# Performance work log

Measured on AMD Instinct MI355X. Metric: run time of the kernel, lower is better.

Reference implementation:

```python
import jax, jax.numpy as jnp
import numpy as np

N_NODES = 100_000
N_EDGES = 1_250_000
IN_FEATS, N_HIDDEN, N_CLASSES = 64, 64, 32


def setup_inputs() -> dict:
    key = jax.random.key(0)
    ks = jax.random.split(key, 8)
    x = jax.random.normal(ks[0], (N_NODES, IN_FEATS), dtype=jnp.float32)
    src = jax.random.randint(ks[1], (N_EDGES,), 0, N_NODES, dtype=jnp.int64)
    dst = jax.random.randint(ks[2], (N_EDGES,), 0, N_NODES, dtype=jnp.int64)
    s1 = 1.0 / np.sqrt(IN_FEATS)
    s2 = 1.0 / np.sqrt(N_HIDDEN)
    W_self1 = jax.random.normal(ks[3], (IN_FEATS, N_HIDDEN), dtype=jnp.float32) * s1
    W_neigh1 = jax.random.normal(ks[4], (IN_FEATS, N_HIDDEN), dtype=jnp.float32) * s1
    b1 = jnp.zeros((N_HIDDEN,), dtype=jnp.float32)
    W_self2 = jax.random.normal(ks[5], (N_HIDDEN, N_CLASSES), dtype=jnp.float32) * s2
    W_neigh2 = jax.random.normal(ks[6], (N_HIDDEN, N_CLASSES), dtype=jnp.float32) * s2
    b2 = jnp.zeros((N_CLASSES,), dtype=jnp.float32)
    return dict(x=x, src=src, dst=dst, W_self1=W_self1, W_neigh1=W_neigh1, b1=b1,
                W_self2=W_self2, W_neigh2=W_neigh2, b2=b2)


def _sage_conv(h, src, dst, W_self, W_neigh, b):
    # mean aggregation over in-neighbors: gather src feats, segment-sum by dst
    n = h.shape[0]
    msg = h[src]  # [E, d] -- dominant memory traffic
    agg = jax.ops.segment_sum(msg, dst, num_segments=n)
    deg = jax.ops.segment_sum(jnp.ones_like(dst, dtype=h.dtype), dst, num_segments=n)
    h_neigh = agg / jnp.maximum(deg, 1.0)[:, None]  # zero-degree nodes get 0 (DGL behavior)
    return h @ W_self + h_neigh @ W_neigh + b


def reference(x, src, dst, W_self1, W_neigh1, b1, W_self2, W_neigh2, b2):
    h = _sage_conv(x, src, dst, W_self1, W_neigh1, b1)
    h = jax.nn.relu(h)
    # dropout(p=0.5) is identity in eval mode
    return _sage_conv(h, src, dst, W_self2, W_neigh2, b2)
```

## Files before the change

### kernel.cpp

```cpp
#include <hip/hip_runtime.h>
#include <hip/hip_bf16.h>


#define NF 64
#define BW 256
#define BSH 8
#define MAXB 512
#define CAPMAX 8192
#define P1_CHUNK 2048
#define H1S 68

typedef __attribute__((ext_vector_type(8))) short short8;
typedef __attribute__((ext_vector_type(8))) unsigned short ushort8v;
typedef __attribute__((ext_vector_type(4))) float floatx4;

__device__ __forceinline__ short bf16hi(float v) {
    __hip_bfloat16 h = __float2bfloat16(v);
    return *(short*)&h;
}
__device__ __forceinline__ float bf2f(short s) {
    __hip_bfloat16 h = *(__hip_bfloat16*)&s;
    return __bfloat162float(h);
}
__device__ __forceinline__ float bits2f(unsigned short u) {
    unsigned int x = ((unsigned int)u) << 16;
    union { unsigned int i; float f; } c; c.i = x; return c.f;
}


__global__ __launch_bounds__(256) void prep_kernel(
        int* __restrict__ gcursor,
        const float* __restrict__ Ws1, const float* __restrict__ Wn1,
        const float* __restrict__ Ws2, const float* __restrict__ Wn2,
        unsigned short* __restrict__ w1p, unsigned short* __restrict__ w2p) {
    const int tid = threadIdx.x;
    if (blockIdx.x == 0) {
        for (int i = tid; i < MAXB; i += 256) gcursor[i] = 0;
        return;
    }
    const int part = blockIdx.x - 1;
    for (int i = tid; i < 32 * 64; i += 256) {
        int n = part * 32 + (i >> 6), k = i & 63;
        float v = (n < 64) ? Ws1[k * 64 + n] : Wn1[k * 64 + (n - 64)];
        short hv = bf16hi(v);
        w1p[n * 64 + k] = (unsigned short)hv;
        w1p[8192 + n * 64 + k] = (unsigned short)bf16hi(v - bf2f(hv));
    }
    for (int i = tid; i < 16 * 64; i += 256) {
        int n = part * 16 + (i >> 6), k = i & 63;
        float v = (n < 32) ? Ws2[k * 32 + n] : Wn2[k * 32 + (n - 32)];
        short hv = bf16hi(v);
        w2p[n * 64 + k] = (unsigned short)hv;
        w2p[4096 + n * 64 + k] = (unsigned short)bf16hi(v - bf2f(hv));
    }
}


__global__ __launch_bounds__(256) void p1_dense1_kernel(
        const int* __restrict__ src, const int* __restrict__ dst,
        int* __restrict__ gcursor, unsigned* __restrict__ bucket,
        int E, int nbuckets, int dblocks,
        const float* __restrict__ X,
        const unsigned short* __restrict__ w1p,
        const float* __restrict__ bias,
        float* __restrict__ outA,
        unsigned short* __restrict__ outB,
        int N) {
    __shared__ int smem_i[2 * MAXB];
    const int tid = threadIdx.x;

    if ((int)blockIdx.x >= dblocks) {
        int* cnt   = smem_i;
        int* cbase = smem_i + MAXB;
        const int bid = blockIdx.x - dblocks;
        const int beg = bid * P1_CHUNK;
        const int end = min(E, beg + P1_CHUNK);
        for (int i = tid; i < nbuckets; i += 256) cnt[i] = 0;
        __syncthreads();
        for (int e = beg + tid; e < end; e += 256)
            atomicAdd(&cnt[dst[e] >> BSH], 1);
        __syncthreads();
        for (int i = tid; i < nbuckets; i += 256) {
            int c = cnt[i];
            cbase[i] = c ? atomicAdd(&gcursor[i], c) : 0;
            cnt[i] = 0;
        }
        __syncthreads();
        for (int e = beg + tid; e < end; e += 256) {
            int d = dst[e];
            int r = d >> BSH;
            int p = cbase[r] + atomicAdd(&cnt[r], 1);
            if (p < CAPMAX)
                bucket[(size_t)r * CAPMAX + p] = ((unsigned)src[e] << BSH) | (unsigned)(d & (BW - 1));
        }
        return;
    }

    constexpr int NT = 8, NSELF = 4;
    const int lane = tid & 63;
    const int wid  = tid >> 6;
    const int m = lane & 15, quad = lane >> 4;
    const int rowblk = blockIdx.x * 128 + wid * 32;

    floatx4 acc[2][NT];
    #pragma unroll
    for (int rt = 0; rt < 2; ++rt)
        #pragma unroll
        for (int t = 0; t < NT; ++t) acc[rt][t] = (floatx4)(0.f);

    short8 ah[2][2], al[2][2];
    #pragma unroll
    for (int rt = 0; rt < 2; ++rt) {
        int r = rowblk + rt * 16 + m;
        if (r >= N) r = N - 1;
        const float* xp = X + (size_t)r * 64 + quad * 8;
        #pragma unroll
        for (int h = 0; h < 2; ++h) {
            floatx4 f0 = *(const floatx4*)(xp + h * 32);
            floatx4 f1 = *(const floatx4*)(xp + h * 32 + 4);
            short8 hi, lo;
            #pragma unroll
            for (int j = 0; j < 4; ++j) {
                short hv = bf16hi(f0[j]);
                hi[j] = hv; lo[j] = bf16hi(f0[j] - bf2f(hv));
                short hv2 = bf16hi(f1[j]);
                hi[4 + j] = hv2; lo[4 + j] = bf16hi(f1[j] - bf2f(hv2));
            }
            ah[rt][h] = hi; al[rt][h] = lo;
        }
    }

    #pragma unroll
    for (int t = 0; t < NT; ++t) {
        int n = t * 16 + m;
        const unsigned short* ph = w1p + n * 64 + quad * 8;
        const unsigned short* pl = ph + 8192;
        #pragma unroll
        for (int h = 0; h < 2; ++h) {
            short8 bh = *(const short8*)(ph + h * 32);
            short8 bl = *(const short8*)(pl + h * 32);
            #pragma unroll
            for (int rt = 0; rt < 2; ++rt) {
                acc[rt][t] = __builtin_amdgcn_mfma_f32_16x16x32_bf16(ah[rt][h], bh, acc[rt][t], 0, 0, 0);
                acc[rt][t] = __builtin_amdgcn_mfma_f32_16x16x32_bf16(al[rt][h], bh, acc[rt][t], 0, 0, 0);
                acc[rt][t] = __builtin_amdgcn_mfma_f32_16x16x32_bf16(ah[rt][h], bl, acc[rt][t], 0, 0, 0);
            }
        }
    }

    #pragma unroll
    for (int rt = 0; rt < 2; ++rt) {
        #pragma unroll
        for (int t = 0; t < NT; ++t) {
            #pragma unroll
            for (int r4 = 0; r4 < 4; ++r4) {
                int row = rowblk + rt * 16 + quad * 4 + r4;
                if (row < N) {
                    if (t < NSELF) {
                        int col = t * 16 + m;
                        outA[(size_t)row * 64 + col] = acc[rt][t][r4] + bias[col];
                    } else {
                        int col = (t - NSELF) * 16 + m;
                        outB[(size_t)row * 64 + col] = (unsigned short)bf16hi(acc[rt][t][r4]);
                    }
                }
            }
        }
    }
}


__global__ __launch_bounds__(256) void p2_csr_kernel(const unsigned* __restrict__ bucket,
                                                     const int* __restrict__ gcursor,
                                                     int* __restrict__ row_start,
                                                     int* __restrict__ csr_src,
                                                     int N, int nbuckets) {
    __shared__ unsigned stage[CAPMAX];
    __shared__ int cnt[BW];
    __shared__ int excl[BW];
    const int r = blockIdx.x;
    const int tid = threadIdx.x;

    int partial = 0;
    for (int i = tid; i < r; i += 256) partial += min(gcursor[i], CAPMAX);
    excl[tid] = partial;
    __syncthreads();
    for (int off = 128; off > 0; off >>= 1) {
        if (tid < off) excl[tid] += excl[tid + off];
        __syncthreads();
    }
    const int base = excl[0];
    const int sz = min(gcursor[r], CAPMAX);
    const unsigned* bsrc = bucket + (size_t)r * CAPMAX;
    __syncthreads();

    cnt[tid] = 0;
    __syncthreads();
    for (int i = tid; i < sz; i += 256) {
        unsigned v = bsrc[i];
        stage[i] = v;
        atomicAdd(&cnt[v & (BW - 1)], 1);
    }
    __syncthreads();
    excl[tid] = cnt[tid];
    __syncthreads();
    for (int off = 1; off < BW; off <<= 1) {
        int v0 = (tid >= off) ? excl[tid - off] : 0;
        __syncthreads();
        excl[tid] += v0;
        __syncthreads();
    }
    int node = r * BW + tid;
    if (node < N) row_start[node] = base + excl[tid] - cnt[tid];
    if (r == nbuckets - 1 && tid == 0) row_start[N] = base + sz;
    __syncthreads();
    cnt[tid] = excl[tid] - cnt[tid];
    __syncthreads();
    for (int i = tid; i < sz; i += 256) {
        unsigned v = stage[i];
        int p = atomicAdd(&cnt[v & (BW - 1)], 1);
        csr_src[base + p] = (int)(v >> BSH);
    }
}


__global__ __launch_bounds__(256) void agg64_d2_kernel(
        const unsigned short* __restrict__ t1n,
        const float* __restrict__ xs,
        const int* __restrict__ row_start,
        const int* __restrict__ csr_src,
        const unsigned short* __restrict__ w2p,
        const float* __restrict__ b2,
        float* __restrict__ outD,
        unsigned short* __restrict__ t2n,
        int N, int E) {
    __shared__ float h1s[16][H1S];
    const int tid = threadIdx.x;
    const int lane = tid & 63;
    const int wid  = tid >> 6;
    const int half = lane >> 5;
    const int g = (lane >> 3) & 3;
    const int c = lane & 7;
    const int nbase = blockIdx.x * 16;

    const int ln0 = wid * 4 + half;
    const int ln1 = ln0 + 2;
    const int n0 = nbase + ln0, n1 = nbase + ln1;
    int beg0 = 0, end0 = 0, beg1 = 0, end1 = 0;
    if (n0 < N) { beg0 = row_start[n0]; end0 = row_start[n0 + 1]; }
    if (n1 < N) { beg1 = row_start[n1]; end1 = row_start[n1 + 1]; }

    float a0[8] = {0.f, 0.f, 0.f, 0.f, 0.f, 0.f, 0.f, 0.f};
    float a1[8] = {0.f, 0.f, 0.f, 0.f, 0.f, 0.f, 0.f, 0.f};
    int j0 = beg0 + g, j1 = beg1 + g;
    const int Em1 = E - 1;
    int i0 = csr_src[min(j0, Em1)];
    int i1 = csr_src[min(j0 + 4, Em1)];
    int i2 = csr_src[min(j1, Em1)];
    int i3 = csr_src[min(j1 + 4, Em1)];
    while ((j0 < end0) || (j1 < end1)) {
        int s0 = ((unsigned)i0 < (unsigned)N) ? i0 : 0;
        int s1 = ((unsigned)i1 < (unsigned)N) ? i1 : 0;
        int s2 = ((unsigned)i2 < (unsigned)N) ? i2 : 0;
        int s3 = ((unsigned)i3 < (unsigned)N) ? i3 : 0;
        ushort8v u0 = *(const ushort8v*)(t1n + (size_t)s0 * 64 + c * 8);
        ushort8v u1 = *(const ushort8v*)(t1n + (size_t)s1 * 64 + c * 8);
        ushort8v u2 = *(const ushort8v*)(t1n + (size_t)s2 * 64 + c * 8);
        ushort8v u3 = *(const ushort8v*)(t1n + (size_t)s3 * 64 + c * 8);
        i0 = csr_src[min(j0 + 8, Em1)];
        i1 = csr_src[min(j0 + 12, Em1)];
        i2 = csr_src[min(j1 + 8, Em1)];
        i3 = csr_src[min(j1 + 12, Em1)];
        const bool c00 = j0 < end0, c01 = j0 + 4 < end0;
        const bool c10 = j1 < end1, c11 = j1 + 4 < end1;
        #pragma unroll
        for (int i = 0; i < 8; ++i) {
            a0[i] += (c00 ? bits2f(u0[i]) : 0.f) + (c01 ? bits2f(u1[i]) : 0.f);
            a1[i] += (c10 ? bits2f(u2[i]) : 0.f) + (c11 ? bits2f(u3[i]) : 0.f);
        }
        j0 += 8; j1 += 8;
    }

    const int m = lane & 15, quad = lane >> 4;
    const int coln = wid * 16 + m;
    const unsigned short* pb = w2p + coln * 64 + quad * 8;
    short8 bhf0 = *(const short8*)(pb);
    short8 bhf1 = *(const short8*)(pb + 32);
    short8 blf0 = *(const short8*)(pb + 4096);
    short8 blf1 = *(const short8*)(pb + 4096 + 32);

    floatx4 x00 = (floatx4)(0.f), x01 = (floatx4)(0.f);
    floatx4 x10 = (floatx4)(0.f), x11 = (floatx4)(0.f);
    if (g == 0) {
        if (n0 < N) {
            const float* p = xs + (size_t)n0 * 64 + c * 8;
            x00 = *(const floatx4*)p; x01 = *(const floatx4*)(p + 4);
        }
        if (n1 < N) {
            const float* p = xs + (size_t)n1 * 64 + c * 8;
            x10 = *(const floatx4*)p; x11 = *(const floatx4*)(p + 4);
        }
    }

    #pragma unroll
    for (int i = 0; i < 8; ++i) {
        float v = a0[i];
        v += __shfl_xor(v, 8);
        v += __shfl_xor(v, 16);
        a0[i] = v;
        float w = a1[i];
        w += __shfl_xor(w, 8);
        w += __shfl_xor(w, 16);
        a1[i] = w;
    }
    if (g == 0) {
        floatx4 h0, h1v;
        if (n0 < N) {
            float invd = 1.0f / fmaxf((float)(end0 - beg0), 1.0f);
            #pragma unroll
            for (int i = 0; i < 4; ++i) {
                h0[i]  = fmaxf(x00[i] + a0[i] * invd, 0.f);
                h1v[i] = fmaxf(x01[i] + a0[4 + i] * invd, 0.f);
            }
        } else { h0 = (floatx4)(0.f); h1v = (floatx4)(0.f); }
        *(floatx4*)&h1s[ln0][c * 8]     = h0;
        *(floatx4*)&h1s[ln0][c * 8 + 4] = h1v;
        if (n1 < N) {
            float invd = 1.0f / fmaxf((float)(end1 - beg1), 1.0f);
            #pragma unroll
            for (int i = 0; i < 4; ++i) {
                h0[i]  = fmaxf(x10[i] + a1[i] * invd, 0.f);
                h1v[i] = fmaxf(x11[i] + a1[4 + i] * invd, 0.f);
            }
        } else { h0 = (floatx4)(0.f); h1v = (floatx4)(0.f); }
        *(floatx4*)&h1s[ln1][c * 8]     = h0;
        *(floatx4*)&h1s[ln1][c * 8 + 4] = h1v;
    }
    __syncthreads();

    short8 ah[2], al[2];
    #pragma unroll
    for (int h = 0; h < 2; ++h) {
        const float* hp = &h1s[m][quad * 8 + h * 32];
        floatx4 f0 = *(const floatx4*)hp;
        floatx4 f1 = *(const floatx4*)(hp + 4);
        short8 hi, lo;
        #pragma unroll
        for (int j = 0; j < 4; ++j) {
            short hv = bf16hi(f0[j]);
            hi[j] = hv; lo[j] = bf16hi(f0[j] - bf2f(hv));
            short hv2 = bf16hi(f1[j]);
            hi[4 + j] = hv2; lo[4 + j] = bf16hi(f1[j] - bf2f(hv2));
        }
        ah[h] = hi; al[h] = lo;
    }
    floatx4 acc2 = (floatx4)(0.f);
    acc2 = __builtin_amdgcn_mfma_f32_16x16x32_bf16(ah[0], bhf0, acc2, 0, 0, 0);
    acc2 = __builtin_amdgcn_mfma_f32_16x16x32_bf16(al[0], bhf0, acc2, 0, 0, 0);
    acc2 = __builtin_amdgcn_mfma_f32_16x16x32_bf16(ah[0], blf0, acc2, 0, 0, 0);
    acc2 = __builtin_amdgcn_mfma_f32_16x16x32_bf16(ah[1], bhf1, acc2, 0, 0, 0);
    acc2 = __builtin_amdgcn_mfma_f32_16x16x32_bf16(al[1], bhf1, acc2, 0, 0, 0);
    acc2 = __builtin_amdgcn_mfma_f32_16x16x32_bf16(ah[1], blf1, acc2, 0, 0, 0);
    #pragma unroll
    for (int r4 = 0; r4 < 4; ++r4) {
        int node = nbase + quad * 4 + r4;
        if (node < N) {
            if (coln < 32) outD[(size_t)node * 32 + coln] = acc2[r4] + b2[coln];
            else t2n[(size_t)node * 32 + (coln - 32)] = (unsigned short)bf16hi(acc2[r4]);
        }
    }
}


__global__ __launch_bounds__(256) void agg32_kernel(float* io,
                                                    const unsigned short* __restrict__ t2n,
                                                    const int* __restrict__ row_start,
                                                    const int* __restrict__ csr_src,
                                                    int N, int E) {
    const int tid = threadIdx.x;
    const int lane = tid & 63;
    const int wid = tid >> 6;
    const int slot = lane >> 4;
    const int g = (lane >> 2) & 3;
    const int c = lane & 3;
    const int n = blockIdx.x * 16 + wid * 4 + slot;

    int beg = 0, end = 0;
    if (n < N) { beg = row_start[n]; end = row_start[n + 1]; }

    floatx4 s0v = (floatx4)(0.f), s1v = (floatx4)(0.f);
    size_t o = (size_t)n * 32 + c * 8;
    if (n < N && g == 0) {
        s0v = *(const floatx4*)(io + o);
        s1v = *(const floatx4*)(io + o + 4);
    }

    float acc[8] = {0.f, 0.f, 0.f, 0.f, 0.f, 0.f, 0.f, 0.f};
    const int Em1 = E - 1;
    for (int j = beg + g; j < end; j += 8) {
        int j2 = j + 4;
        int s0 = csr_src[j];
        int s1 = csr_src[min(j2, Em1)];
        s0 = ((unsigned)s0 < (unsigned)N) ? s0 : 0;
        s1 = ((unsigned)s1 < (unsigned)N) ? s1 : 0;
        ushort8v u0 = *(const ushort8v*)(t2n + (size_t)s0 * 32 + c * 8);
        ushort8v u1 = *(const ushort8v*)(t2n + (size_t)s1 * 32 + c * 8);
        const bool c1 = j2 < end;
        #pragma unroll
        for (int i = 0; i < 8; ++i)
            acc[i] += bits2f(u0[i]) + (c1 ? bits2f(u1[i]) : 0.f);
    }
    #pragma unroll
    for (int i = 0; i < 8; ++i) {
        float v = acc[i];
        v += __shfl_xor(v, 4);
        v += __shfl_xor(v, 8);
        acc[i] = v;
    }
    if (n < N && g == 0) {
        float inv = 1.0f / fmaxf((float)(end - beg), 1.0f);
        floatx4 r0, r1;
        #pragma unroll
        for (int i = 0; i < 4; ++i) {
            r0[i] = s0v[i] + acc[i] * inv;
            r1[i] = s1v[i] + acc[4 + i] * inv;
        }
        *(floatx4*)(io + o) = r0;
        *(floatx4*)(io + o + 4) = r1;
    }
}


__global__ __launch_bounds__(256) void deg_kernel(const int* __restrict__ dst,
                                                  float* __restrict__ deg, int E) {
    int e = blockIdx.x * blockDim.x + threadIdx.x;
    if (e < E) atomicAdd(&deg[dst[e]], 1.0f);
}

__global__ __launch_bounds__(256) void agg_atomic_kernel(const float* __restrict__ feats,
                                                         const int* __restrict__ src,
                                                         const int* __restrict__ dst,
                                                         float* __restrict__ agg, int E) {
    int tid = blockIdx.x * blockDim.x + threadIdx.x;
    if (tid >= E * NF) return;
    int e = tid >> 6, f = tid & 63;
    atomicAdd(&agg[(size_t)dst[e] * NF + f], feats[(size_t)src[e] * NF + f]);
}

__global__ __launch_bounds__(256) void layer1_fb_kernel(const float* __restrict__ x,
                                                        const float* __restrict__ agg,
                                                        const float* __restrict__ deg,
                                                        const float* __restrict__ Wself,
                                                        const float* __restrict__ Wneigh,
                                                        const float* __restrict__ b,
                                                        float* __restrict__ h1, int N) {
    int tid = blockIdx.x * blockDim.x + threadIdx.x;
    if (tid >= N * NF) return;
    int n = tid >> 6, c = tid & 63;
    float inv = 1.0f / fmaxf(deg[n], 1.0f);
    const float* xrow = x + (size_t)n * NF;
    const float* arow = agg + (size_t)n * NF;
    float acc = b[c];
    #pragma unroll
    for (int k = 0; k < NF; ++k) {
        acc += xrow[k] * Wself[k * NF + c];
        acc += (arow[k] * inv) * Wneigh[k * NF + c];
    }
    h1[tid] = fmaxf(acc, 0.f);
}

__global__ __launch_bounds__(256) void layer2_fb_kernel(const float* __restrict__ h1,
                                                        const float* __restrict__ agg,
                                                        const float* __restrict__ deg,
                                                        const float* __restrict__ Wself,
                                                        const float* __restrict__ Wneigh,
                                                        const float* __restrict__ b,
                                                        float* __restrict__ out, int N) {
    int tid = blockIdx.x * blockDim.x + threadIdx.x;
    if (tid >= N * 32) return;
    int n = tid >> 5, c = tid & 31;
    float inv = 1.0f / fmaxf(deg[n], 1.0f);
    const float* hrow = h1 + (size_t)n * NF;
    const float* arow = agg + (size_t)n * NF;
    float acc = b[c];
    #pragma unroll
    for (int k = 0; k < NF; ++k) {
        acc += hrow[k] * Wself[k * 32 + c];
        acc += (arow[k] * inv) * Wneigh[k * 32 + c];
    }
    out[tid] = acc;
}


extern "C" void kernel_launch(void* const* d_in, const int* in_sizes, int n_in,
                              void* d_out, int out_size, void* d_ws, size_t ws_size,
                              hipStream_t stream) {
    const float* x        = (const float*)d_in[0];
    const int*   src      = (const int*)d_in[1];
    const int*   dst      = (const int*)d_in[2];
    const float* W_self1  = (const float*)d_in[3];
    const float* W_neigh1 = (const float*)d_in[4];
    const float* b1       = (const float*)d_in[5];
    const float* W_self2  = (const float*)d_in[6];
    const float* W_neigh2 = (const float*)d_in[7];
    const float* b2       = (const float*)d_in[8];
    float* out = (float*)d_out;

    const int N = in_sizes[0] / NF;
    const int E = in_sizes[1];
    const int nbuckets = (N + BW - 1) / BW;

    const size_t rsPad = ((size_t)N + 8) & ~7ull;
    int* gcursor   = (int*)d_ws;
    unsigned short* w2p = (unsigned short*)(gcursor + MAXB);
    unsigned short* w1p = w2p + 8192;
    int* row_start = (int*)(w1p + 16384);
    int* csr_src   = row_start + rsPad;
    uintptr_t pa = (uintptr_t)(csr_src + (((size_t)E + 7) & ~7ull));
    pa = (pa + 127) & ~(uintptr_t)127;
    float* bufA = (float*)pa;
    unsigned* bucket = (unsigned*)bufA;
    unsigned short* t1n = (unsigned short*)(bufA + (size_t)N * NF);
    unsigned short* t2n = t1n + (size_t)N * NF;
    size_t need = (size_t)((char*)(t2n + (size_t)N * 32) - (char*)d_ws);

    bool fast = ws_size >= need
             && E > 0
             && nbuckets <= MAXB
             && (size_t)nbuckets * CAPMAX <= (size_t)N * NF
             && (size_t)E * 2 / (size_t)nbuckets <= CAPMAX
             && N < (1 << 24)
             && out_size >= N * 32;

    if (fast) {
        prep_kernel<<<5, 256, 0, stream>>>(gcursor, W_self1, W_neigh1,
                                           W_self2, W_neigh2, w1p, w2p);
        int dblocks  = (N + 127) / 128;
        int p1blocks = (E + P1_CHUNK - 1) / P1_CHUNK;
        unsigned* bucket2 = (unsigned*)(t2n + (((size_t)N * 32 + 63) & ~63ull));
        size_t need2 = (size_t)((char*)(bucket2 + (size_t)nbuckets * CAPMAX) - (char*)d_ws);
        if (ws_size >= need2) {
            p1_dense1_kernel<<<dblocks + p1blocks, 256, 0, stream>>>(
                src, dst, gcursor, bucket2, E, nbuckets, dblocks,
                x, w1p, b1, bufA, t1n, N);
            p2_csr_kernel<<<nbuckets, 256, 0, stream>>>(bucket2, gcursor,
                                                        row_start, csr_src, N, nbuckets);
        } else {
            p1_dense1_kernel<<<p1blocks, 256, 0, stream>>>(
                src, dst, gcursor, bucket, E, nbuckets, 0,
                x, w1p, b1, bufA, t1n, N);
            p2_csr_kernel<<<nbuckets, 256, 0, stream>>>(bucket, gcursor,
                                                        row_start, csr_src, N, nbuckets);
            p1_dense1_kernel<<<dblocks, 256, 0, stream>>>(
                src, dst, gcursor, bucket, E, nbuckets, dblocks,
                x, w1p, b1, bufA, t1n, N);
        }
        agg64_d2_kernel<<<(N + 15) / 16, 256, 0, stream>>>(
            t1n, bufA, row_start, csr_src, w2p, b2, out, t2n, N, E);
        agg32_kernel<<<(N + 15) / 16, 256, 0, stream>>>(out, t2n,
                                                        row_start, csr_src, N, E);
    } else {
        float* deg = (float*)d_ws;
        float* agg = deg + N;
        float* h1  = agg + (size_t)N * NF;
        hipMemsetAsync(deg, 0, (size_t)(N + (size_t)N * NF) * sizeof(float), stream);
        deg_kernel<<<(E + 255) / 256, 256, 0, stream>>>(dst, deg, E);
        int at = E * NF;
        agg_atomic_kernel<<<(at + 255) / 256, 256, 0, stream>>>(x, src, dst, agg, E);
        layer1_fb_kernel<<<(N * NF + 255) / 256, 256, 0, stream>>>(x, agg, deg, W_self1,
                                                                   W_neigh1, b1, h1, N);
        hipMemsetAsync(agg, 0, (size_t)N * NF * sizeof(float), stream);
        agg_atomic_kernel<<<(at + 255) / 256, 256, 0, stream>>>(h1, src, dst, agg, E);
        layer2_fb_kernel<<<(N * 32 + 255) / 256, 256, 0, stream>>>(h1, agg, deg, W_self2,
                                                                   W_neigh2, b2, out, N);
    }
}
```

Measured before the change: 203.6 us.

## Fuse weight packing into layer-1 kernel and deepen gather unrolling

```diff
diff --git a/kernel.cpp b/kernel.cpp
--- a/kernel.cpp
+++ b/kernel.cpp
@@ -28,46 +28,34 @@
 }
 
 
-__global__ __launch_bounds__(256) void prep_kernel(
-        int* __restrict__ gcursor,
-        const float* __restrict__ Ws1, const float* __restrict__ Wn1,
-        const float* __restrict__ Ws2, const float* __restrict__ Wn2,
-        unsigned short* __restrict__ w1p, unsigned short* __restrict__ w2p) {
-    const int tid = threadIdx.x;
-    if (blockIdx.x == 0) {
-        for (int i = tid; i < MAXB; i += 256) gcursor[i] = 0;
-        return;
-    }
-    const int part = blockIdx.x - 1;
-    for (int i = tid; i < 32 * 64; i += 256) {
-        int n = part * 32 + (i >> 6), k = i & 63;
-        float v = (n < 64) ? Ws1[k * 64 + n] : Wn1[k * 64 + (n - 64)];
-        short hv = bf16hi(v);
-        w1p[n * 64 + k] = (unsigned short)hv;
-        w1p[8192 + n * 64 + k] = (unsigned short)bf16hi(v - bf2f(hv));
-    }
-    for (int i = tid; i < 16 * 64; i += 256) {
-        int n = part * 16 + (i >> 6), k = i & 63;
-        float v = (n < 32) ? Ws2[k * 32 + n] : Wn2[k * 32 + (n - 32)];
-        short hv = bf16hi(v);
-        w2p[n * 64 + k] = (unsigned short)hv;
-        w2p[4096 + n * 64 + k] = (unsigned short)bf16hi(v - bf2f(hv));
-    }
-}
-
-
-__global__ __launch_bounds__(256) void p1_dense1_kernel(
+__global__ __launch_bounds__(256) void d1p1_kernel(
         const int* __restrict__ src, const int* __restrict__ dst,
         int* __restrict__ gcursor, unsigned* __restrict__ bucket,
-        int E, int nbuckets, int dblocks,
+        int E, int nbuckets, int dblocks, int packBase,
         const float* __restrict__ X,
-        const unsigned short* __restrict__ w1p,
+        const float* __restrict__ Wself,
+        const float* __restrict__ Wneigh,
         const float* __restrict__ bias,
         float* __restrict__ outA,
         unsigned short* __restrict__ outB,
-        int N) {
-    __shared__ int smem_i[2 * MAXB];
+        int N,
+        const float* __restrict__ Ws2,
+        const float* __restrict__ Wn2,
+        unsigned short* __restrict__ w2p) {
+    __shared__ __align__(16) int smem_i[9216];
     const int tid = threadIdx.x;
+
+    if ((int)blockIdx.x >= packBase) {
+        const int part = blockIdx.x - packBase;
+        for (int i = tid; i < 16 * 64; i += 256) {
+            int n = part * 16 + (i >> 6), k = i & 63;
+            float v = (n < 32) ? Ws2[k * 32 + n] : Wn2[k * 32 + (n - 32)];
+            short hv = bf16hi(v);
+            w2p[n * 64 + k] = (unsigned short)hv;
+            w2p[4096 + n * 64 + k] = (unsigned short)bf16hi(v - bf2f(hv));
+        }
+        return;
+    }
 
     if ((int)blockIdx.x >= dblocks) {
         int* cnt   = smem_i;
@@ -96,7 +84,17 @@
         return;
     }
 
-    constexpr int NT = 8, NSELF = 4;
+    constexpr int NT = 8, NSELF = 4, NO = 128, HALF = 64;
+    unsigned short* wh = (unsigned short*)smem_i;
+    unsigned short* wl = wh + NO * 72;
+    for (int i = tid; i < NO * 64; i += 256) {
+        int n = i & (NO - 1), k = i / NO;
+        float v = (n < HALF) ? Wself[k * HALF + n] : Wneigh[k * HALF + (n - HALF)];
+        short hv = bf16hi(v);
+        wh[n * 72 + k] = (unsigned short)hv;
+        wl[n * 72 + k] = (unsigned short)bf16hi(v - bf2f(hv));
+    }
+
     const int lane = tid & 63;
     const int wid  = tid >> 6;
     const int m = lane & 15, quad = lane >> 4;
@@ -129,12 +127,13 @@
             ah[rt][h] = hi; al[rt][h] = lo;
         }
     }
+    __syncthreads();
 
     #pragma unroll
     for (int t = 0; t < NT; ++t) {
         int n = t * 16 + m;
-        const unsigned short* ph = w1p + n * 64 + quad * 8;
-        const unsigned short* pl = ph + 8192;
+        const unsigned short* ph = wh + n * 72 + quad * 8;
+        const unsigned short* pl = wl + n * 72 + quad * 8;
         #pragma unroll
         for (int h = 0; h < 2; ++h) {
             short8 bh = *(const short8*)(ph + h * 32);
@@ -256,29 +255,39 @@
     const int Em1 = E - 1;
     int i0 = csr_src[min(j0, Em1)];
     int i1 = csr_src[min(j0 + 4, Em1)];
-    int i2 = csr_src[min(j1, Em1)];
-    int i3 = csr_src[min(j1 + 4, Em1)];
+    int i2 = csr_src[min(j0 + 8, Em1)];
+    int i3 = csr_src[min(j1, Em1)];
+    int i4 = csr_src[min(j1 + 4, Em1)];
+    int i5 = csr_src[min(j1 + 8, Em1)];
     while ((j0 < end0) || (j1 < end1)) {
         int s0 = ((unsigned)i0 < (unsigned)N) ? i0 : 0;
         int s1 = ((unsigned)i1 < (unsigned)N) ? i1 : 0;
         int s2 = ((unsigned)i2 < (unsigned)N) ? i2 : 0;
         int s3 = ((unsigned)i3 < (unsigned)N) ? i3 : 0;
+        int s4 = ((unsigned)i4 < (unsigned)N) ? i4 : 0;
+        int s5 = ((unsigned)i5 < (unsigned)N) ? i5 : 0;
         ushort8v u0 = *(const ushort8v*)(t1n + (size_t)s0 * 64 + c * 8);
         ushort8v u1 = *(const ushort8v*)(t1n + (size_t)s1 * 64 + c * 8);
         ushort8v u2 = *(const ushort8v*)(t1n + (size_t)s2 * 64 + c * 8);
         ushort8v u3 = *(const ushort8v*)(t1n + (size_t)s3 * 64 + c * 8);
-        i0 = csr_src[min(j0 + 8, Em1)];
-        i1 = csr_src[min(j0 + 12, Em1)];
-        i2 = csr_src[min(j1 + 8, Em1)];
+        ushort8v u4 = *(const ushort8v*)(t1n + (size_t)s4 * 64 + c * 8);
+        ushort8v u5 = *(const ushort8v*)(t1n + (size_t)s5 * 64 + c * 8);
+        i0 = csr_src[min(j0 + 12, Em1)];
+        i1 = csr_src[min(j0 + 16, Em1)];
+        i2 = csr_src[min(j0 + 20, Em1)];
         i3 = csr_src[min(j1 + 12, Em1)];
-        const bool c00 = j0 < end0, c01 = j0 + 4 < end0;
-        const bool c10 = j1 < end1, c11 = j1 + 4 < end1;
+        i4 = csr_src[min(j1 + 16, Em1)];
+        i5 = csr_src[min(j1 + 20, Em1)];
+        const bool c00 = j0 < end0, c01 = j0 + 4 < end0, c02 = j0 + 8 < end0;
+        const bool c10 = j1 < end1, c11 = j1 + 4 < end1, c12 = j1 + 8 < end1;
         #pragma unroll
         for (int i = 0; i < 8; ++i) {
-            a0[i] += (c00 ? bits2f(u0[i]) : 0.f) + (c01 ? bits2f(u1[i]) : 0.f);
-            a1[i] += (c10 ? bits2f(u2[i]) : 0.f) + (c11 ? bits2f(u3[i]) : 0.f);
-        }
-        j0 += 8; j1 += 8;
+            a0[i] += (c00 ? bits2f(u0[i]) : 0.f) + (c01 ? bits2f(u1[i]) : 0.f)
+                   + (c02 ? bits2f(u2[i]) : 0.f);
+            a1[i] += (c10 ? bits2f(u3[i]) : 0.f) + (c11 ? bits2f(u4[i]) : 0.f)
+                   + (c12 ? bits2f(u5[i]) : 0.f);
+        }
+        j0 += 12; j1 += 12;
     }
 
     const int m = lane & 15, quad = lane >> 4;
@@ -397,18 +406,21 @@
 
     float acc[8] = {0.f, 0.f, 0.f, 0.f, 0.f, 0.f, 0.f, 0.f};
     const int Em1 = E - 1;
-    for (int j = beg + g; j < end; j += 8) {
-        int j2 = j + 4;
+    for (int j = beg + g; j < end; j += 12) {
         int s0 = csr_src[j];
-        int s1 = csr_src[min(j2, Em1)];
+        int s1 = csr_src[min(j + 4, Em1)];
+        int s2 = csr_src[min(j + 8, Em1)];
         s0 = ((unsigned)s0 < (unsigned)N) ? s0 : 0;
         s1 = ((unsigned)s1 < (unsigned)N) ? s1 : 0;
+        s2 = ((unsigned)s2 < (unsigned)N) ? s2 : 0;
         ushort8v u0 = *(const ushort8v*)(t2n + (size_t)s0 * 32 + c * 8);
         ushort8v u1 = *(const ushort8v*)(t2n + (size_t)s1 * 32 + c * 8);
-        const bool c1 = j2 < end;
+        ushort8v u2 = *(const ushort8v*)(t2n + (size_t)s2 * 32 + c * 8);
+        const bool c1 = j + 4 < end, c2 = j + 8 < end;
         #pragma unroll
         for (int i = 0; i < 8; ++i)
-            acc[i] += bits2f(u0[i]) + (c1 ? bits2f(u1[i]) : 0.f);
+            acc[i] += bits2f(u0[i]) + (c1 ? bits2f(u1[i]) : 0.f)
+                    + (c2 ? bits2f(u2[i]) : 0.f);
     }
     #pragma unroll
     for (int i = 0; i < 8; ++i) {
@@ -513,8 +525,7 @@
     const size_t rsPad = ((size_t)N + 8) & ~7ull;
     int* gcursor   = (int*)d_ws;
     unsigned short* w2p = (unsigned short*)(gcursor + MAXB);
-    unsigned short* w1p = w2p + 8192;
-    int* row_start = (int*)(w1p + 16384);
+    int* row_start = (int*)(w2p + 8192);
     int* csr_src   = row_start + rsPad;
     uintptr_t pa = (uintptr_t)(csr_src + (((size_t)E + 7) & ~7ull));
     pa = (pa + 127) & ~(uintptr_t)127;
@@ -525,7 +536,7 @@
     size_t need = (size_t)((char*)(t2n + (size_t)N * 32) - (char*)d_ws);
 
     bool fast = ws_size >= need
-             && E > 0
+             && E > 0 && N > 0
              && nbuckets <= MAXB
              && (size_t)nbuckets * CAPMAX <= (size_t)N * NF
              && (size_t)E * 2 / (size_t)nbuckets <= CAPMAX
@@ -533,27 +544,31 @@
              && out_size >= N * 32;
 
     if (fast) {
-        prep_kernel<<<5, 256, 0, stream>>>(gcursor, W_self1, W_neigh1,
-                                           W_self2, W_neigh2, w1p, w2p);
-        int dblocks  = (N + 127) / 128;
-        int p1blocks = (E + P1_CHUNK - 1) / P1_CHUNK;
+        const int dblocks  = (N + 127) / 128;
+        const int p1blocks = (E + P1_CHUNK - 1) / P1_CHUNK;
         unsigned* bucket2 = (unsigned*)(t2n + (((size_t)N * 32 + 63) & ~63ull));
         size_t need2 = (size_t)((char*)(bucket2 + (size_t)nbuckets * CAPMAX) - (char*)d_ws);
+        hipMemsetAsync(gcursor, 0, MAXB * sizeof(int), stream);
         if (ws_size >= need2) {
-            p1_dense1_kernel<<<dblocks + p1blocks, 256, 0, stream>>>(
+            d1p1_kernel<<<dblocks + p1blocks + 4, 256, 0, stream>>>(
                 src, dst, gcursor, bucket2, E, nbuckets, dblocks,
-                x, w1p, b1, bufA, t1n, N);
+                dblocks + p1blocks,
+                x, W_self1, W_neigh1, b1, bufA, t1n, N,
+                W_self2, W_neigh2, w2p);
             p2_csr_kernel<<<nbuckets, 256, 0, stream>>>(bucket2, gcursor,
                                                         row_start, csr_src, N, nbuckets);
         } else {
-            p1_dense1_kernel<<<p1blocks, 256, 0, stream>>>(
-                src, dst, gcursor, bucket, E, nbuckets, 0,
-                x, w1p, b1, bufA, t1n, N);
+            d1p1_kernel<<<p1blocks + 4, 256, 0, stream>>>(
+                src, dst, gcursor, bucket, E, nbuckets, 0, p1blocks,
+                x, W_self1, W_neigh1, b1, bufA, t1n, N,
+                W_self2, W_neigh2, w2p);
             p2_csr_kernel<<<nbuckets, 256, 0, stream>>>(bucket, gcursor,
                                                         row_start, csr_src, N, nbuckets);
-            p1_dense1_kernel<<<dblocks, 256, 0, stream>>>(
+            d1p1_kernel<<<dblocks, 256, 0, stream>>>(
                 src, dst, gcursor, bucket, E, nbuckets, dblocks,
-                x, w1p, b1, bufA, t1n, N);
+                dblocks + p1blocks,
+                x, W_self1, W_neigh1, b1, bufA, t1n, N,
+                W_self2, W_neigh2, w2p);
         }
         agg64_d2_kernel<<<(N + 15) / 16, 256, 0, stream>>>(
             t1n, bufA, row_start, csr_src, w2p, b2, out, t2n, N, E);
```

New measurement: 190.7 us. 6.3% less time.
